# Kernel tuning notes

Hardware: AMD Instinct MI355X
Metric: run time of the kernel (lower is better)

Reference implementation:

```python
import jax, jax.numpy as jnp
import numpy as np

EPS = 1e-8

def setup_inputs() -> dict:
    key = jax.random.key(0)
    k1, k2, k3 = jax.random.split(key, 3)
    b, c, h, w = 64, 20, 128, 128
    x = jax.random.normal(k1, (b, c, h, w), dtype=jnp.float32)
    y = jax.random.randint(k2, (b, c), 0, 2).astype(jnp.int32)
    threshold_p = jnp.zeros((b, c, h * w), dtype=jnp.float32)
    fg = jax.random.uniform(k3, (b, c), dtype=jnp.float32)
    return {"x": x, "y": y, "threshold_p": threshold_p, "fg": fg, "iter": 0}

def reference(x, y, threshold_p, fg, iter):
    b, c, h, w = x.shape
    hw = h * w
    xs = jax.nn.sigmoid(x.reshape(b, c, hw))  # [b,c,hw]
    yf = y.astype(xs.dtype)
    if iter % 100 < 80:
        # per-row descending sort, pick the fg*(h*w)-th value as threshold
        srt = -jnp.sort(-xs.reshape(b * c, hw), axis=1)  # descending
        idx = (fg.reshape(-1) * hw).astype(jnp.int32)  # [b*c]
        thr = jnp.take_along_axis(srt, idx[:, None], axis=1).reshape(b, c, 1)
        thr = jax.lax.stop_gradient(thr)
    else:
        thr = jax.nn.sigmoid(jnp.mean(threshold_p.reshape(b, c, hw), axis=2))[:, :, None]
        xs = jax.lax.stop_gradient(xs)
    thr = jnp.clip(thr, 0.0001)  # [b,c,1], broadcasts over hw
    y_ = yf[:, :, None]  # [b,c,1] broadcast equivalent of stacking hw copies
    mask_low = jax.lax.stop_gradient((xs <= thr).astype(xs.dtype) * y_)
    mask_high = jax.lax.stop_gradient((xs > thr).astype(xs.dtype) * y_)
    h_low = (-(xs * xs) / (thr * thr) + 2.0 * xs / thr) * mask_low
    alpha = 1.0 / jnp.clip((1.0 - thr) ** 2, EPS)
    h_high = alpha * (1.0 - xs) * (1.0 - 2.0 * thr + xs) * mask_high
    if iter % 100 < 80:
        neg_loss = -(1.0 - y_) * jnp.log(jnp.clip(1.0 - xs, EPS))
        loss = jnp.mean(h_high + h_low + neg_loss)
    else:
        loss = jnp.sum(h_low) / jnp.sum(mask_low) + jnp.sum(h_high) / jnp.sum(mask_high)
    return loss
```

## Files before the change

kernel.cpp:

```cpp
#include <hip/hip_runtime.h>

#define HW     16384
#define NROWS  1280
#define NT     512
#define NWAVES (NT / 64)
#define CAP    1024
#define NBIN1  4096

__device__ __forceinline__ unsigned f2u(float f) {
    unsigned u = __float_as_uint(f);
    unsigned m = (unsigned)((int)u >> 31);
    return u ^ (m | 0x80000000u);
}
__device__ __forceinline__ float u2f(unsigned u) {
    u = (u & 0x80000000u) ? (u & 0x7fffffffu) : ~u;
    return __uint_as_float(u);
}

__device__ __forceinline__ void block_scan_pick(
    const unsigned* h, int bpl, int stride, unsigned kk,
    volatile unsigned* s_bin, volatile unsigned* s_k, unsigned* wtot)
{
    const int tid  = threadIdx.x;
    const int lane = tid & 63;
    const int wid  = tid >> 6;
    const int base = tid * bpl;
    unsigned local = 0;
    for (int j = 0; j < bpl; ++j) {
        int b = base + j;
        local += h[stride * b] + (stride == 2 ? h[stride * b + 1] : 0u);
    }
    unsigned s = local;
    #pragma unroll
    for (int off = 1; off < 64; off <<= 1) {
        unsigned t = __shfl_down(s, off, 64);
        if (lane + off < 64) s += t;
    }
    if (lane == 0) wtot[wid] = s;
    __syncthreads();
    unsigned aw = 0;
    #pragma unroll
    for (int w = 0; w < NWAVES; ++w) if (w > wid) aw += wtot[w];
    const unsigned above = aw + (s - local);
    if (above <= kk && above + local > kk) {
        unsigned run = above;
        for (int j = bpl - 1; j >= 0; --j) {
            int b = base + j;
            unsigned c = h[stride * b] + (stride == 2 ? h[stride * b + 1] : 0u);
            if (run + c > kk) { *s_bin = (unsigned)b; *s_k = kk - run; break; }
            run += c;
        }
    }
    __syncthreads();
}

__global__ __launch_bounds__(NT) void spatial_bce_row(
    const float* __restrict__ x, const int* __restrict__ y,
    const float* __restrict__ fg, double* __restrict__ partial)
{
    __shared__ unsigned hist[NBIN1 * 2];
    __shared__ unsigned buf[CAP];
    __shared__ unsigned wtot[NWAVES];
    __shared__ unsigned s_cnt, s_bin, s_k;
    __shared__ float    swf[NWAVES][5];
    __shared__ double   swd[NWAVES];

    const int row  = blockIdx.x;
    const int tid  = threadIdx.x;
    const int lane = tid & 63;
    const int wid  = tid >> 6;
    const float4* x4 = (const float4*)(x + (size_t)row * HW);
    const float L2E   = 1.44269504f;
    const float LN2   = 0.69314718f;
    const float NLCAP = 18.420680744f;

    const int yrow = y[row];

    if (yrow == 0) {
        float a0 = 0.f, a1 = 0.f, a2 = 0.f, a3 = 0.f;
        for (int i = tid; i < HW / 4; i += NT) {
            float4 v = x4[i];
            a0 += fminf(fmaxf(v.x, 0.f) + LN2 * log2f(1.f + exp2f(-L2E * fabsf(v.x))), NLCAP);
            a1 += fminf(fmaxf(v.y, 0.f) + LN2 * log2f(1.f + exp2f(-L2E * fabsf(v.y))), NLCAP);
            a2 += fminf(fmaxf(v.z, 0.f) + LN2 * log2f(1.f + exp2f(-L2E * fabsf(v.z))), NLCAP);
            a3 += fminf(fmaxf(v.w, 0.f) + LN2 * log2f(1.f + exp2f(-L2E * fabsf(v.w))), NLCAP);
        }
        double acc = (double)((a0 + a1) + (a2 + a3));
        #pragma unroll
        for (int off = 32; off > 0; off >>= 1) acc += __shfl_down(acc, off, 64);
        if (lane == 0) swd[wid] = acc;
        __syncthreads();
        if (tid == 0) {
            double t = 0.0;
            for (int w = 0; w < NWAVES; ++w) t += swd[w];
            partial[row] = t;
        }
        return;
    }

    {
        uint4 z = {0u, 0u, 0u, 0u};
        for (int i = tid; i < NBIN1 * 2 / 4; i += NT) ((uint4*)hist)[i] = z;
    }
    if (tid == 0) {
        int k = (int)(fg[row] * (float)HW);
        k = max(0, min(HW - 1, k));
        s_k = (unsigned)k; s_cnt = 0u;
    }
    __syncthreads();
    const unsigned k0 = s_k;

    const int rep = tid & 1;
    for (int i = tid; i < HW / 4; i += 2 * NT) {
        float4 v0 = x4[i];
        float4 v1 = x4[i + NT];
        atomicAdd(&hist[2 * (f2u(v0.x) >> 20) + rep], 1u);
        atomicAdd(&hist[2 * (f2u(v0.y) >> 20) + rep], 1u);
        atomicAdd(&hist[2 * (f2u(v0.z) >> 20) + rep], 1u);
        atomicAdd(&hist[2 * (f2u(v0.w) >> 20) + rep], 1u);
        atomicAdd(&hist[2 * (f2u(v1.x) >> 20) + rep], 1u);
        atomicAdd(&hist[2 * (f2u(v1.y) >> 20) + rep], 1u);
        atomicAdd(&hist[2 * (f2u(v1.z) >> 20) + rep], 1u);
        atomicAdd(&hist[2 * (f2u(v1.w) >> 20) + rep], 1u);
    }
    __syncthreads();
    block_scan_pick(hist, NBIN1 / NT, 2, k0, &s_bin, &s_k, wtot);
    const unsigned bin1 = s_bin;
    const unsigned k1   = s_k;

    for (int i = tid; i < 2048; i += NT) hist[i] = 0u;
    float sLa = 0.f, s2La = 0.f, sHa = 0.f, s2Ha = 0.f;
    float sLb = 0.f, s2Lb = 0.f, sHb = 0.f, s2Hb = 0.f;
    int   nH = 0;
    for (int i = tid; i < HW / 4; i += 2 * NT) {
        float4 v0 = x4[i];
        float4 v1 = x4[i + NT];
        float e0[4] = {v0.x, v0.y, v0.z, v0.w};
        float e1[4] = {v1.x, v1.y, v1.z, v1.w};
        #pragma unroll
        for (int j = 0; j < 4; ++j) {
            float xv = e0[j];
            unsigned u = f2u(xv);
            unsigned b = u >> 20;
            if (b == bin1) {
                unsigned p = atomicAdd(&s_cnt, 1u);
                if (p < CAP) buf[p] = u;
            } else {
                float s = __builtin_amdgcn_rcpf(1.f + exp2f(-L2E * xv));
                float s2 = s * s;
                if (b > bin1) { sHa += s; s2Ha += s2; ++nH; }
                else          { sLa += s; s2La += s2; }
            }
        }
        #pragma unroll
        for (int j = 0; j < 4; ++j) {
            float xv = e1[j];
            unsigned u = f2u(xv);
            unsigned b = u >> 20;
            if (b == bin1) {
                unsigned p = atomicAdd(&s_cnt, 1u);
                if (p < CAP) buf[p] = u;
            } else {
                float s = __builtin_amdgcn_rcpf(1.f + exp2f(-L2E * xv));
                float s2 = s * s;
                if (b > bin1) { sHb += s; s2Hb += s2; ++nH; }
                else          { sLb += s; s2Lb += s2; }
            }
        }
    }
    float sL = sLa + sLb, s2L = s2La + s2Lb;
    float sH = sHa + sHb, s2H = s2Ha + s2Hb;
    __syncthreads();
    const unsigned cnt = s_cnt;

    unsigned ustar;
    if (cnt <= CAP) {
        for (int c = tid; c < (int)cnt; c += NT)
            atomicAdd(&hist[(buf[c] >> 10) & 1023u], 1u);
        __syncthreads();
        block_scan_pick(hist, 1024 / NT, 1, k1, &s_bin, &s_k, wtot);
        const unsigned pfx22 = (bin1 << 10) | s_bin;
        const unsigned k2    = s_k;
        for (int c = tid; c < (int)cnt; c += NT)
            if ((buf[c] >> 10) == pfx22) atomicAdd(&hist[1024 + (buf[c] & 1023u)], 1u);
        __syncthreads();
        block_scan_pick(hist + 1024, 1024 / NT, 1, k2, &s_bin, &s_k, wtot);
        ustar = (pfx22 << 10) | s_bin;
    } else {
        for (int i = tid; i < HW / 4; i += NT) {
            float4 v = x4[i];
            unsigned u[4] = {f2u(v.x), f2u(v.y), f2u(v.z), f2u(v.w)};
            #pragma unroll
            for (int j = 0; j < 4; ++j)
                if ((u[j] >> 20) == bin1) atomicAdd(&hist[(u[j] >> 10) & 1023u], 1u);
        }
        __syncthreads();
        block_scan_pick(hist, 1024 / NT, 1, k1, &s_bin, &s_k, wtot);
        const unsigned pfx22 = (bin1 << 10) | s_bin;
        const unsigned k2    = s_k;
        for (int i = tid; i < HW / 4; i += NT) {
            float4 v = x4[i];
            unsigned u[4] = {f2u(v.x), f2u(v.y), f2u(v.z), f2u(v.w)};
            #pragma unroll
            for (int j = 0; j < 4; ++j)
                if ((u[j] >> 10) == pfx22) atomicAdd(&hist[1024 + (u[j] & 1023u)], 1u);
        }
        __syncthreads();
        block_scan_pick(hist + 1024, 1024 / NT, 1, k2, &s_bin, &s_k, wtot);
        ustar = (pfx22 << 10) | s_bin;
    }

    const float xk = u2f(ustar);
    float thr = 1.0f / (1.0f + expf(-xk));
    thr = fmaxf(thr, 1e-4f);

    if (cnt <= CAP) {
        for (int c = tid; c < (int)cnt; c += NT) {
            float xv = u2f(buf[c]);
            float s  = __builtin_amdgcn_rcpf(1.f + exp2f(-L2E * xv));
            float s2 = s * s;
            if (s > thr) { sH += s; s2H += s2; ++nH; }
            else         { sL += s; s2L += s2; }
        }
    } else {
        for (int i = tid; i < HW / 4; i += NT) {
            float4 v = x4[i];
            float e[4] = {v.x, v.y, v.z, v.w};
            #pragma unroll
            for (int j = 0; j < 4; ++j) {
                unsigned u = f2u(e[j]);
                if ((u >> 20) == bin1) {
                    float s  = __builtin_amdgcn_rcpf(1.f + exp2f(-L2E * e[j]));
                    float s2 = s * s;
                    if (s > thr) { sH += s; s2H += s2; ++nH; }
                    else         { sL += s; s2L += s2; }
                }
            }
        }
    }

    float nHf = (float)nH;
    #pragma unroll
    for (int off = 32; off > 0; off >>= 1) {
        sL  += __shfl_down(sL,  off, 64);
        s2L += __shfl_down(s2L, off, 64);
        sH  += __shfl_down(sH,  off, 64);
        s2H += __shfl_down(s2H, off, 64);
        nHf += __shfl_down(nHf, off, 64);
    }
    if (lane == 0) {
        swf[wid][0] = sL; swf[wid][1] = s2L; swf[wid][2] = sH;
        swf[wid][3] = s2H; swf[wid][4] = nHf;
    }
    __syncthreads();
    if (tid == 0) {
        double SL = 0, S2L = 0, SH = 0, S2H = 0, NH = 0;
        for (int w = 0; w < NWAVES; ++w) {
            SL += swf[w][0]; S2L += swf[w][1]; SH += swf[w][2];
            S2H += swf[w][3]; NH += (double)swf[w][4];
        }
        const double t   = (double)thr;
        const double omt = 1.0 - t;
        const double al  = 1.0 / fmax(omt * omt, 1e-8);
        partial[row] = 2.0 * SL / t - S2L / (t * t)
                     + al * (NH * (1.0 - 2.0 * t) + 2.0 * t * SH - S2H);
    }
}

__global__ __launch_bounds__(256) void spatial_bce_final(
    const double* __restrict__ partial, float* __restrict__ out)
{
    __shared__ double sred[256];
    double acc = 0.0;
    for (int i = threadIdx.x; i < NROWS; i += 256) acc += partial[i];
    sred[threadIdx.x] = acc;
    __syncthreads();
    for (int off = 128; off > 0; off >>= 1) {
        if (threadIdx.x < off) sred[threadIdx.x] += sred[threadIdx.x + off];
        __syncthreads();
    }
    if (threadIdx.x == 0)
        out[0] = (float)(sred[0] / ((double)NROWS * (double)HW));
}

extern "C" void kernel_launch(void* const* d_in, const int* in_sizes, int n_in,
                              void* d_out, int out_size, void* d_ws, size_t ws_size,
                              hipStream_t stream) {
    const float* x  = (const float*)d_in[0];
    const int*   y  = (const int*)d_in[1];
    const float* fg = (const float*)d_in[3];

    double* partial = (double*)d_ws;

    spatial_bce_row<<<NROWS, NT, 0, stream>>>(x, y, fg, partial);
    spatial_bce_final<<<1, 256, 0, stream>>>(partial, (float*)d_out);
}
```

Before: 38.24 us.

## Predict top-k threshold window from Gaussian quantile to skip the histogram pass

For rows with y=1, the coarse 4096-bin histogram pass is replaced by an analytic guess of the k-th order statistic, assuming normal data, via an inverse-normal approximation with a 6-sigma window. One fused pass now accumulates total sigmoid sums, the sums above the window, and counts above and below it, and buffers the in-window candidates. The exact threshold is then found with a small fine histogram and a rank-select over a second buffer. Totals are used to derive the low-side sums. If the window misses k or overflows the buffer, it falls back to the exact radix-select over the whole row, which costs more when the data is not Gaussian-like.

After: 38.38 us. About the same (+0.3%).

```diff
diff --git a/kernel.cpp b/kernel.cpp
--- a/kernel.cpp
+++ b/kernel.cpp
@@ -4,8 +4,8 @@
 #define NROWS  1280
 #define NT     512
 #define NWAVES (NT / 64)
-#define CAP    1024
-#define NBIN1  4096
+#define CAP    1536
+#define MAXB   128
 
 __device__ __forceinline__ unsigned f2u(float f) {
     unsigned u = __float_as_uint(f);
@@ -17,8 +17,37 @@
     return __uint_as_float(u);
 }
 
+__device__ __forceinline__ float norminv(float p) {
+    const float a1=-3.969683028665376e+01f,a2=2.209460984245205e+02f,
+                a3=-2.759285104469687e+02f,a4=1.383577518672690e+02f,
+                a5=-3.066479806614716e+01f,a6=2.506628277459239e+00f;
+    const float b1=-5.447609879822406e+01f,b2=1.615858368580409e+02f,
+                b3=-1.556989798598866e+02f,b4=6.680131188771972e+01f,
+                b5=-1.328068155288572e+01f;
+    const float c1=-7.784894002430293e-03f,c2=-3.223964580411365e-01f,
+                c3=-2.400758277161838e+00f,c4=-2.549732539343734e+00f,
+                c5=4.374664141464968e+00f,c6=2.938163982698783e+00f;
+    const float d1=7.784695709041462e-03f,d2=3.224671290700398e-01f,
+                d3=2.445134137142996e+00f,d4=3.754408661907416e+00f;
+    const float plow = 0.02425f;
+    float q, r;
+    if (p < plow) {
+        q = sqrtf(-2.f * logf(p));
+        return (((((c1*q+c2)*q+c3)*q+c4)*q+c5)*q+c6) /
+               ((((d1*q+d2)*q+d3)*q+d4)*q+1.f);
+    } else if (p <= 1.f - plow) {
+        q = p - 0.5f; r = q * q;
+        return (((((a1*r+a2)*r+a3)*r+a4)*r+a5)*r+a6)*q /
+               (((((b1*r+b2)*r+b3)*r+b4)*r+b5)*r+1.f);
+    } else {
+        q = sqrtf(-2.f * logf(1.f - p));
+        return -(((((c1*q+c2)*q+c3)*q+c4)*q+c5)*q+c6) /
+                ((((d1*q+d2)*q+d3)*q+d4)*q+1.f);
+    }
+}
+
 __device__ __forceinline__ void block_scan_pick(
-    const unsigned* h, int bpl, int stride, unsigned kk,
+    const unsigned* h, int bpl, unsigned kk,
     volatile unsigned* s_bin, volatile unsigned* s_k, unsigned* wtot)
 {
     const int tid  = threadIdx.x;
@@ -26,10 +55,7 @@
     const int wid  = tid >> 6;
     const int base = tid * bpl;
     unsigned local = 0;
-    for (int j = 0; j < bpl; ++j) {
-        int b = base + j;
-        local += h[stride * b] + (stride == 2 ? h[stride * b + 1] : 0u);
-    }
+    for (int j = 0; j < bpl; ++j) local += h[base + j];
     unsigned s = local;
     #pragma unroll
     for (int off = 1; off < 64; off <<= 1) {
@@ -45,9 +71,8 @@
     if (above <= kk && above + local > kk) {
         unsigned run = above;
         for (int j = bpl - 1; j >= 0; --j) {
-            int b = base + j;
-            unsigned c = h[stride * b] + (stride == 2 ? h[stride * b + 1] : 0u);
-            if (run + c > kk) { *s_bin = (unsigned)b; *s_k = kk - run; break; }
+            unsigned c = h[base + j];
+            if (run + c > kk) { *s_bin = (unsigned)(base + j); *s_k = kk - run; break; }
             run += c;
         }
     }
@@ -58,11 +83,12 @@
     const float* __restrict__ x, const int* __restrict__ y,
     const float* __restrict__ fg, double* __restrict__ partial)
 {
-    __shared__ unsigned hist[NBIN1 * 2];
+    __shared__ unsigned hist[4096];
     __shared__ unsigned buf[CAP];
+    __shared__ unsigned buf2[MAXB];
     __shared__ unsigned wtot[NWAVES];
-    __shared__ unsigned s_cnt, s_bin, s_k;
-    __shared__ float    swf[NWAVES][5];
+    __shared__ unsigned s_cnt, s_cnt2, s_bin, s_k, s_val;
+    __shared__ float    swf[NWAVES][6];
     __shared__ double   swd[NWAVES];
 
     const int row  = blockIdx.x;
@@ -98,40 +124,26 @@
         return;
     }
 
+    int k = (int)(fg[row] * (float)HW);
+    k = max(0, min(HW - 1, k));
+    const unsigned ku = (unsigned)k;
+    const float pq  = 1.f - ((float)k + 0.5f) * (1.f / (float)HW);
+    const float z   = norminv(pq);
+    const float phi = 0.39894228f * exp2f(-0.72134752f * z * z);
+    const float sig = sqrtf(pq * (1.f - pq) * (1.f / (float)HW)) / phi;
+    const float dl  = 6.f * sig + 0.02f;
+    const float fa  = z + dl, fb = z - dl;
+    const unsigned ua = f2u(fa), ub = f2u(fb);
+
     {
-        uint4 z = {0u, 0u, 0u, 0u};
-        for (int i = tid; i < NBIN1 * 2 / 4; i += NT) ((uint4*)hist)[i] = z;
-    }
-    if (tid == 0) {
-        int k = (int)(fg[row] * (float)HW);
-        k = max(0, min(HW - 1, k));
-        s_k = (unsigned)k; s_cnt = 0u;
-    }
-    __syncthreads();
-    const unsigned k0 = s_k;
-
-    const int rep = tid & 1;
-    for (int i = tid; i < HW / 4; i += 2 * NT) {
-        float4 v0 = x4[i];
-        float4 v1 = x4[i + NT];
-        atomicAdd(&hist[2 * (f2u(v0.x) >> 20) + rep], 1u);
-        atomicAdd(&hist[2 * (f2u(v0.y) >> 20) + rep], 1u);
-        atomicAdd(&hist[2 * (f2u(v0.z) >> 20) + rep], 1u);
-        atomicAdd(&hist[2 * (f2u(v0.w) >> 20) + rep], 1u);
-        atomicAdd(&hist[2 * (f2u(v1.x) >> 20) + rep], 1u);
-        atomicAdd(&hist[2 * (f2u(v1.y) >> 20) + rep], 1u);
-        atomicAdd(&hist[2 * (f2u(v1.z) >> 20) + rep], 1u);
-        atomicAdd(&hist[2 * (f2u(v1.w) >> 20) + rep], 1u);
-    }
-    __syncthreads();
-    block_scan_pick(hist, NBIN1 / NT, 2, k0, &s_bin, &s_k, wtot);
-    const unsigned bin1 = s_bin;
-    const unsigned k1   = s_k;
-
-    for (int i = tid; i < 2048; i += NT) hist[i] = 0u;
-    float sLa = 0.f, s2La = 0.f, sHa = 0.f, s2Ha = 0.f;
-    float sLb = 0.f, s2Lb = 0.f, sHb = 0.f, s2Hb = 0.f;
-    int   nH = 0;
+        uint4 zz = {0u, 0u, 0u, 0u};
+        for (int i = tid; i < 1024 / 4; i += NT) ((uint4*)hist)[i] = zz;
+    }
+    if (tid == 0) { s_cnt = 0u; s_cnt2 = 0u; }
+    __syncthreads();
+
+    float t1a = 0.f, t2a = 0.f, gaa = 0.f, g2aa = 0.f, cafa = 0.f, cbfa = 0.f;
+    float t1b = 0.f, t2b = 0.f, gab = 0.f, g2ab = 0.f, cafb = 0.f, cbfb = 0.f;
     for (int i = tid; i < HW / 4; i += 2 * NT) {
         float4 v0 = x4[i];
         float4 v1 = x4[i + NT];
@@ -141,52 +153,151 @@
         for (int j = 0; j < 4; ++j) {
             float xv = e0[j];
             unsigned u = f2u(xv);
-            unsigned b = u >> 20;
-            if (b == bin1) {
-                unsigned p = atomicAdd(&s_cnt, 1u);
-                if (p < CAP) buf[p] = u;
-            } else {
-                float s = __builtin_amdgcn_rcpf(1.f + exp2f(-L2E * xv));
-                float s2 = s * s;
-                if (b > bin1) { sHa += s; s2Ha += s2; ++nH; }
-                else          { sLa += s; s2La += s2; }
+            float s = __builtin_amdgcn_rcpf(1.f + exp2f(-L2E * xv));
+            float s2 = s * s;
+            t1a += s; t2a += s2;
+            if (u > ua) { gaa += s; g2aa += s2; cafa += 1.f; }
+            if (u > ub) {
+                cbfa += 1.f;
+                if (u <= ua) { unsigned p = atomicAdd(&s_cnt, 1u); if (p < CAP) buf[p] = u; }
             }
         }
         #pragma unroll
         for (int j = 0; j < 4; ++j) {
             float xv = e1[j];
             unsigned u = f2u(xv);
-            unsigned b = u >> 20;
-            if (b == bin1) {
-                unsigned p = atomicAdd(&s_cnt, 1u);
-                if (p < CAP) buf[p] = u;
-            } else {
-                float s = __builtin_amdgcn_rcpf(1.f + exp2f(-L2E * xv));
-                float s2 = s * s;
-                if (b > bin1) { sHb += s; s2Hb += s2; ++nH; }
-                else          { sLb += s; s2Lb += s2; }
-            }
-        }
-    }
-    float sL = sLa + sLb, s2L = s2La + s2Lb;
-    float sH = sHa + sHb, s2H = s2Ha + s2Hb;
-    __syncthreads();
+            float s = __builtin_amdgcn_rcpf(1.f + exp2f(-L2E * xv));
+            float s2 = s * s;
+            t1b += s; t2b += s2;
+            if (u > ua) { gab += s; g2ab += s2; cafb += 1.f; }
+            if (u > ub) {
+                cbfb += 1.f;
+                if (u <= ua) { unsigned p = atomicAdd(&s_cnt, 1u); if (p < CAP) buf[p] = u; }
+            }
+        }
+    }
+    float t1 = t1a + t1b, t2 = t2a + t2b;
+    float ga = gaa + gab, g2a = g2aa + g2ab;
+    float caf = cafa + cafb, cbf = cbfa + cbfb;
+    #pragma unroll
+    for (int off = 32; off > 0; off >>= 1) {
+        t1  += __shfl_down(t1,  off, 64);
+        t2  += __shfl_down(t2,  off, 64);
+        ga  += __shfl_down(ga,  off, 64);
+        g2a += __shfl_down(g2a, off, 64);
+        caf += __shfl_down(caf, off, 64);
+        cbf += __shfl_down(cbf, off, 64);
+    }
+    if (lane == 0) {
+        swf[wid][0] = t1;  swf[wid][1] = t2;  swf[wid][2] = ga;
+        swf[wid][3] = g2a; swf[wid][4] = caf; swf[wid][5] = cbf;
+    }
+    __syncthreads();
+    double dS1 = 0, dS2 = 0, dGa = 0, dG2a = 0, dCa = 0, dCb = 0;
+    #pragma unroll
+    for (int w = 0; w < NWAVES; ++w) {
+        dS1 += swf[w][0]; dS2 += swf[w][1]; dGa  += swf[w][2];
+        dG2a += swf[w][3]; dCa += swf[w][4]; dCb += swf[w][5];
+    }
+    const unsigned ca  = (unsigned)(dCa + 0.5);
+    const unsigned cb  = (unsigned)(dCb + 0.5);
     const unsigned cnt = s_cnt;
+    const unsigned UCLIP = f2u(-9.2102404f);
+    const bool valid = (ca <= ku) && (ku < cb) && (cnt <= CAP);
 
     unsigned ustar;
-    if (cnt <= CAP) {
-        for (int c = tid; c < (int)cnt; c += NT)
-            atomicAdd(&hist[(buf[c] >> 10) & 1023u], 1u);
-        __syncthreads();
-        block_scan_pick(hist, 1024 / NT, 1, k1, &s_bin, &s_k, wtot);
-        const unsigned pfx22 = (bin1 << 10) | s_bin;
-        const unsigned k2    = s_k;
-        for (int c = tid; c < (int)cnt; c += NT)
-            if ((buf[c] >> 10) == pfx22) atomicAdd(&hist[1024 + (buf[c] & 1023u)], 1u);
-        __syncthreads();
-        block_scan_pick(hist + 1024, 1024 / NT, 1, k2, &s_bin, &s_k, wtot);
-        ustar = (pfx22 << 10) | s_bin;
+    bool addSide;
+    float hs = 0.f, hs2 = 0.f, hn = 0.f;
+
+    if (valid) {
+        const float scale = 1024.f / (fa - fb);
+        for (int c = tid; c < (int)cnt; c += NT) {
+            float xv = u2f(buf[c]);
+            int bn = (int)((xv - fb) * scale);
+            bn = max(0, min(1023, bn));
+            atomicAdd(&hist[bn], 1u);
+        }
+        __syncthreads();
+        const unsigned kp = ku - ca;
+        block_scan_pick(hist, 1024 / NT, kp, &s_bin, &s_k, wtot);
+        const unsigned binv = s_bin;
+        const unsigned kin  = s_k;
+        for (int c = tid; c < (int)cnt; c += NT) {
+            unsigned u = buf[c];
+            float xv = u2f(u);
+            int bn = (int)((xv - fb) * scale);
+            bn = max(0, min(1023, bn));
+            if (bn == (int)binv) { unsigned p = atomicAdd(&s_cnt2, 1u); if (p < MAXB) buf2[p] = u; }
+        }
+        __syncthreads();
+        const unsigned m = s_cnt2;
+        if (m <= MAXB) {
+            for (int i = tid; i < (int)m; i += NT) {
+                unsigned v = buf2[i];
+                unsigned gt = 0, eq = 0;
+                for (int j = 0; j < (int)m; ++j) {
+                    unsigned w = buf2[j];
+                    gt += (w > v); eq += (w == v);
+                }
+                if (gt <= kin && kin < gt + eq) s_val = v;
+            }
+        } else {
+            for (int c = tid; c < (int)cnt; c += NT) {
+                unsigned v = buf[c];
+                unsigned gt = 0, eq = 0;
+                for (int j = 0; j < (int)cnt; ++j) {
+                    unsigned w = buf[j];
+                    gt += (w > v); eq += (w == v);
+                }
+                if (gt <= kp && kp < gt + eq) s_val = v;
+            }
+        }
+        __syncthreads();
+        ustar = s_val;
+
+        if (ustar >= UCLIP) {
+            addSide = true;
+            for (int c = tid; c < (int)cnt; c += NT) {
+                unsigned u = buf[c];
+                if (u > ustar) {
+                    float xv = u2f(u);
+                    float s = __builtin_amdgcn_rcpf(1.f + exp2f(-L2E * xv));
+                    hs += s; hs2 += s * s; hn += 1.f;
+                }
+            }
+        } else {
+            addSide = false;
+            for (int i = tid; i < HW / 4; i += NT) {
+                float4 v = x4[i];
+                float e[4] = {v.x, v.y, v.z, v.w};
+                #pragma unroll
+                for (int j = 0; j < 4; ++j) {
+                    if (f2u(e[j]) > UCLIP) {
+                        float s = __builtin_amdgcn_rcpf(1.f + exp2f(-L2E * e[j]));
+                        hs += s; hs2 += s * s; hn += 1.f;
+                    }
+                }
+            }
+        }
     } else {
+        {
+            uint4 zz = {0u, 0u, 0u, 0u};
+            for (int i = tid; i < 4096 / 4; i += NT) ((uint4*)hist)[i] = zz;
+        }
+        __syncthreads();
+        for (int i = tid; i < HW / 4; i += NT) {
+            float4 v = x4[i];
+            atomicAdd(&hist[f2u(v.x) >> 20], 1u);
+            atomicAdd(&hist[f2u(v.y) >> 20], 1u);
+            atomicAdd(&hist[f2u(v.z) >> 20], 1u);
+            atomicAdd(&hist[f2u(v.w) >> 20], 1u);
+        }
+        __syncthreads();
+        block_scan_pick(hist, 4096 / NT, ku, &s_bin, &s_k, wtot);
+        const unsigned bin1 = s_bin;
+        const unsigned k1   = s_k;
+        for (int i = tid; i < 2048; i += NT) hist[i] = 0u;
+        __syncthreads();
         for (int i = tid; i < HW / 4; i += NT) {
             float4 v = x4[i];
             unsigned u[4] = {f2u(v.x), f2u(v.y), f2u(v.z), f2u(v.w)};
@@ -195,7 +306,7 @@
                 if ((u[j] >> 20) == bin1) atomicAdd(&hist[(u[j] >> 10) & 1023u], 1u);
         }
         __syncthreads();
-        block_scan_pick(hist, 1024 / NT, 1, k1, &s_bin, &s_k, wtot);
+        block_scan_pick(hist, 1024 / NT, k1, &s_bin, &s_k, wtot);
         const unsigned pfx22 = (bin1 << 10) | s_bin;
         const unsigned k2    = s_k;
         for (int i = tid; i < HW / 4; i += NT) {
@@ -206,60 +317,46 @@
                 if ((u[j] >> 10) == pfx22) atomicAdd(&hist[1024 + (u[j] & 1023u)], 1u);
         }
         __syncthreads();
-        block_scan_pick(hist + 1024, 1024 / NT, 1, k2, &s_bin, &s_k, wtot);
+        block_scan_pick(hist + 1024, 1024 / NT, k2, &s_bin, &s_k, wtot);
         ustar = (pfx22 << 10) | s_bin;
-    }
-
-    const float xk = u2f(ustar);
-    float thr = 1.0f / (1.0f + expf(-xk));
-    thr = fmaxf(thr, 1e-4f);
-
-    if (cnt <= CAP) {
-        for (int c = tid; c < (int)cnt; c += NT) {
-            float xv = u2f(buf[c]);
-            float s  = __builtin_amdgcn_rcpf(1.f + exp2f(-L2E * xv));
-            float s2 = s * s;
-            if (s > thr) { sH += s; s2H += s2; ++nH; }
-            else         { sL += s; s2L += s2; }
-        }
-    } else {
+
+        addSide = false;
+        const unsigned uthr = max(ustar, UCLIP);
         for (int i = tid; i < HW / 4; i += NT) {
             float4 v = x4[i];
             float e[4] = {v.x, v.y, v.z, v.w};
             #pragma unroll
             for (int j = 0; j < 4; ++j) {
-                unsigned u = f2u(e[j]);
-                if ((u >> 20) == bin1) {
-                    float s  = __builtin_amdgcn_rcpf(1.f + exp2f(-L2E * e[j]));
-                    float s2 = s * s;
-                    if (s > thr) { sH += s; s2H += s2; ++nH; }
-                    else         { sL += s; s2L += s2; }
-                }
-            }
-        }
-    }
-
-    float nHf = (float)nH;
+                if (f2u(e[j]) > uthr) {
+                    float s = __builtin_amdgcn_rcpf(1.f + exp2f(-L2E * e[j]));
+                    hs += s; hs2 += s * s; hn += 1.f;
+                }
+            }
+        }
+    }
+
     #pragma unroll
     for (int off = 32; off > 0; off >>= 1) {
-        sL  += __shfl_down(sL,  off, 64);
-        s2L += __shfl_down(s2L, off, 64);
-        sH  += __shfl_down(sH,  off, 64);
-        s2H += __shfl_down(s2H, off, 64);
-        nHf += __shfl_down(nHf, off, 64);
-    }
-    if (lane == 0) {
-        swf[wid][0] = sL; swf[wid][1] = s2L; swf[wid][2] = sH;
-        swf[wid][3] = s2H; swf[wid][4] = nHf;
-    }
+        hs  += __shfl_down(hs,  off, 64);
+        hs2 += __shfl_down(hs2, off, 64);
+        hn  += __shfl_down(hn,  off, 64);
+    }
+    if (lane == 0) { swf[wid][0] = hs; swf[wid][1] = hs2; swf[wid][2] = hn; }
     __syncthreads();
     if (tid == 0) {
-        double SL = 0, S2L = 0, SH = 0, S2H = 0, NH = 0;
+        double HS = 0, HS2 = 0, HN = 0;
         for (int w = 0; w < NWAVES; ++w) {
-            SL += swf[w][0]; S2L += swf[w][1]; SH += swf[w][2];
-            S2H += swf[w][3]; NH += (double)swf[w][4];
-        }
-        const double t   = (double)thr;
+            HS += swf[w][0]; HS2 += swf[w][1]; HN += swf[w][2];
+        }
+        double SH, S2H, NH;
+        if (addSide) { SH = dGa + HS; S2H = dG2a + HS2; NH = dCa + HN; }
+        else         { SH = HS;       S2H = HS2;        NH = HN; }
+        const double SL = dS1 - SH, S2L = dS2 - S2H;
+
+        const float xk = u2f(ustar);
+        float thrf = 1.0f / (1.0f + expf(-xk));
+        thrf = fmaxf(thrf, 1e-4f);
+        const double t   = (double)thrf;
         const double omt = 1.0 - t;
         const double al  = 1.0 / fmax(omt * omt, 1e-8);
         partial[row] = 2.0 * SL / t - S2L / (t * t)
```

## Fuse final reduction via last-block counter and unroll row loads by four

Applied to the files above, without the earlier changes.

Removes the separate final reduction kernel: each row block increments a global done counter after a fence, and the last block to finish sums all partials and writes the output. A memset of the counter is added to the stream before the launch. Separately, the load loops in the negative-row, histogram and classification passes now issue four float4 loads per iteration instead of one or two, for more memory-level parallelism. The trade is a small memset launch in place of the second kernel, plus higher register pressure from the unrolling.

Result: slower. 70.55 us (+84.5%).

```diff
diff --git a/kernel.cpp b/kernel.cpp
--- a/kernel.cpp
+++ b/kernel.cpp
@@ -56,12 +56,13 @@
 
 __global__ __launch_bounds__(NT) void spatial_bce_row(
     const float* __restrict__ x, const int* __restrict__ y,
-    const float* __restrict__ fg, double* __restrict__ partial)
+    const float* __restrict__ fg, double* __restrict__ partial,
+    unsigned* __restrict__ done, float* __restrict__ out)
 {
     __shared__ unsigned hist[NBIN1 * 2];
     __shared__ unsigned buf[CAP];
     __shared__ unsigned wtot[NWAVES];
-    __shared__ unsigned s_cnt, s_bin, s_k;
+    __shared__ unsigned s_cnt, s_bin, s_k, s_last;
     __shared__ float    swf[NWAVES][5];
     __shared__ double   swd[NWAVES];
 
@@ -78,12 +79,27 @@
 
     if (yrow == 0) {
         float a0 = 0.f, a1 = 0.f, a2 = 0.f, a3 = 0.f;
-        for (int i = tid; i < HW / 4; i += NT) {
-            float4 v = x4[i];
-            a0 += fminf(fmaxf(v.x, 0.f) + LN2 * log2f(1.f + exp2f(-L2E * fabsf(v.x))), NLCAP);
-            a1 += fminf(fmaxf(v.y, 0.f) + LN2 * log2f(1.f + exp2f(-L2E * fabsf(v.y))), NLCAP);
-            a2 += fminf(fmaxf(v.z, 0.f) + LN2 * log2f(1.f + exp2f(-L2E * fabsf(v.z))), NLCAP);
-            a3 += fminf(fmaxf(v.w, 0.f) + LN2 * log2f(1.f + exp2f(-L2E * fabsf(v.w))), NLCAP);
+        for (int i = tid; i < HW / 4; i += 4 * NT) {
+            float4 v0 = x4[i];
+            float4 v1 = x4[i + NT];
+            float4 v2 = x4[i + 2 * NT];
+            float4 v3 = x4[i + 3 * NT];
+            a0 += fminf(fmaxf(v0.x, 0.f) + LN2 * log2f(1.f + exp2f(-L2E * fabsf(v0.x))), NLCAP);
+            a1 += fminf(fmaxf(v0.y, 0.f) + LN2 * log2f(1.f + exp2f(-L2E * fabsf(v0.y))), NLCAP);
+            a2 += fminf(fmaxf(v0.z, 0.f) + LN2 * log2f(1.f + exp2f(-L2E * fabsf(v0.z))), NLCAP);
+            a3 += fminf(fmaxf(v0.w, 0.f) + LN2 * log2f(1.f + exp2f(-L2E * fabsf(v0.w))), NLCAP);
+            a0 += fminf(fmaxf(v1.x, 0.f) + LN2 * log2f(1.f + exp2f(-L2E * fabsf(v1.x))), NLCAP);
+            a1 += fminf(fmaxf(v1.y, 0.f) + LN2 * log2f(1.f + exp2f(-L2E * fabsf(v1.y))), NLCAP);
+            a2 += fminf(fmaxf(v1.z, 0.f) + LN2 * log2f(1.f + exp2f(-L2E * fabsf(v1.z))), NLCAP);
+            a3 += fminf(fmaxf(v1.w, 0.f) + LN2 * log2f(1.f + exp2f(-L2E * fabsf(v1.w))), NLCAP);
+            a0 += fminf(fmaxf(v2.x, 0.f) + LN2 * log2f(1.f + exp2f(-L2E * fabsf(v2.x))), NLCAP);
+            a1 += fminf(fmaxf(v2.y, 0.f) + LN2 * log2f(1.f + exp2f(-L2E * fabsf(v2.y))), NLCAP);
+            a2 += fminf(fmaxf(v2.z, 0.f) + LN2 * log2f(1.f + exp2f(-L2E * fabsf(v2.z))), NLCAP);
+            a3 += fminf(fmaxf(v2.w, 0.f) + LN2 * log2f(1.f + exp2f(-L2E * fabsf(v2.w))), NLCAP);
+            a0 += fminf(fmaxf(v3.x, 0.f) + LN2 * log2f(1.f + exp2f(-L2E * fabsf(v3.x))), NLCAP);
+            a1 += fminf(fmaxf(v3.y, 0.f) + LN2 * log2f(1.f + exp2f(-L2E * fabsf(v3.y))), NLCAP);
+            a2 += fminf(fmaxf(v3.z, 0.f) + LN2 * log2f(1.f + exp2f(-L2E * fabsf(v3.z))), NLCAP);
+            a3 += fminf(fmaxf(v3.w, 0.f) + LN2 * log2f(1.f + exp2f(-L2E * fabsf(v3.w))), NLCAP);
         }
         double acc = (double)((a0 + a1) + (a2 + a3));
         #pragma unroll
@@ -95,192 +111,209 @@
             for (int w = 0; w < NWAVES; ++w) t += swd[w];
             partial[row] = t;
         }
-        return;
-    }
-
-    {
-        uint4 z = {0u, 0u, 0u, 0u};
-        for (int i = tid; i < NBIN1 * 2 / 4; i += NT) ((uint4*)hist)[i] = z;
-    }
-    if (tid == 0) {
-        int k = (int)(fg[row] * (float)HW);
-        k = max(0, min(HW - 1, k));
-        s_k = (unsigned)k; s_cnt = 0u;
-    }
-    __syncthreads();
-    const unsigned k0 = s_k;
-
-    const int rep = tid & 1;
-    for (int i = tid; i < HW / 4; i += 2 * NT) {
-        float4 v0 = x4[i];
-        float4 v1 = x4[i + NT];
-        atomicAdd(&hist[2 * (f2u(v0.x) >> 20) + rep], 1u);
-        atomicAdd(&hist[2 * (f2u(v0.y) >> 20) + rep], 1u);
-        atomicAdd(&hist[2 * (f2u(v0.z) >> 20) + rep], 1u);
-        atomicAdd(&hist[2 * (f2u(v0.w) >> 20) + rep], 1u);
-        atomicAdd(&hist[2 * (f2u(v1.x) >> 20) + rep], 1u);
-        atomicAdd(&hist[2 * (f2u(v1.y) >> 20) + rep], 1u);
-        atomicAdd(&hist[2 * (f2u(v1.z) >> 20) + rep], 1u);
-        atomicAdd(&hist[2 * (f2u(v1.w) >> 20) + rep], 1u);
-    }
-    __syncthreads();
-    block_scan_pick(hist, NBIN1 / NT, 2, k0, &s_bin, &s_k, wtot);
-    const unsigned bin1 = s_bin;
-    const unsigned k1   = s_k;
-
-    for (int i = tid; i < 2048; i += NT) hist[i] = 0u;
-    float sLa = 0.f, s2La = 0.f, sHa = 0.f, s2Ha = 0.f;
-    float sLb = 0.f, s2Lb = 0.f, sHb = 0.f, s2Hb = 0.f;
-    int   nH = 0;
-    for (int i = tid; i < HW / 4; i += 2 * NT) {
-        float4 v0 = x4[i];
-        float4 v1 = x4[i + NT];
-        float e0[4] = {v0.x, v0.y, v0.z, v0.w};
-        float e1[4] = {v1.x, v1.y, v1.z, v1.w};
+    } else {
+        {
+            uint4 z = {0u, 0u, 0u, 0u};
+            for (int i = tid; i < NBIN1 * 2 / 4; i += NT) ((uint4*)hist)[i] = z;
+        }
+        if (tid == 0) {
+            int k = (int)(fg[row] * (float)HW);
+            k = max(0, min(HW - 1, k));
+            s_k = (unsigned)k; s_cnt = 0u;
+        }
+        __syncthreads();
+        const unsigned k0 = s_k;
+
+        const int rep = tid & 1;
+        for (int i = tid; i < HW / 4; i += 4 * NT) {
+            float4 v0 = x4[i];
+            float4 v1 = x4[i + NT];
+            float4 v2 = x4[i + 2 * NT];
+            float4 v3 = x4[i + 3 * NT];
+            atomicAdd(&hist[2 * (f2u(v0.x) >> 20) + rep], 1u);
+            atomicAdd(&hist[2 * (f2u(v0.y) >> 20) + rep], 1u);
+            atomicAdd(&hist[2 * (f2u(v0.z) >> 20) + rep], 1u);
+            atomicAdd(&hist[2 * (f2u(v0.w) >> 20) + rep], 1u);
+            atomicAdd(&hist[2 * (f2u(v1.x) >> 20) + rep], 1u);
+            atomicAdd(&hist[2 * (f2u(v1.y) >> 20) + rep], 1u);
+            atomicAdd(&hist[2 * (f2u(v1.z) >> 20) + rep], 1u);
+            atomicAdd(&hist[2 * (f2u(v1.w) >> 20) + rep], 1u);
+            atomicAdd(&hist[2 * (f2u(v2.x) >> 20) + rep], 1u);
+            atomicAdd(&hist[2 * (f2u(v2.y) >> 20) + rep], 1u);
+            atomicAdd(&hist[2 * (f2u(v2.z) >> 20) + rep], 1u);
+            atomicAdd(&hist[2 * (f2u(v2.w) >> 20) + rep], 1u);
+            atomicAdd(&hist[2 * (f2u(v3.x) >> 20) + rep], 1u);
+            atomicAdd(&hist[2 * (f2u(v3.y) >> 20) + rep], 1u);
+            atomicAdd(&hist[2 * (f2u(v3.z) >> 20) + rep], 1u);
+            atomicAdd(&hist[2 * (f2u(v3.w) >> 20) + rep], 1u);
+        }
+        __syncthreads();
+        block_scan_pick(hist, NBIN1 / NT, 2, k0, &s_bin, &s_k, wtot);
+        const unsigned bin1 = s_bin;
+        const unsigned k1   = s_k;
+
+        for (int i = tid; i < 2048; i += NT) hist[i] = 0u;
+        float sLa = 0.f, s2La = 0.f, sHa = 0.f, s2Ha = 0.f;
+        float sLb = 0.f, s2Lb = 0.f, sHb = 0.f, s2Hb = 0.f;
+        int   nH = 0;
+        for (int i = tid; i < HW / 4; i += 4 * NT) {
+            float4 v0 = x4[i];
+            float4 v1 = x4[i + NT];
+            float4 v2 = x4[i + 2 * NT];
+            float4 v3 = x4[i + 3 * NT];
+            float e0[8] = {v0.x, v0.y, v0.z, v0.w, v1.x, v1.y, v1.z, v1.w};
+            float e1[8] = {v2.x, v2.y, v2.z, v2.w, v3.x, v3.y, v3.z, v3.w};
+            #pragma unroll
+            for (int j = 0; j < 8; ++j) {
+                float xv = e0[j];
+                unsigned u = f2u(xv);
+                unsigned b = u >> 20;
+                if (b == bin1) {
+                    unsigned p = atomicAdd(&s_cnt, 1u);
+                    if (p < CAP) buf[p] = u;
+                } else {
+                    float s = __builtin_amdgcn_rcpf(1.f + exp2f(-L2E * xv));
+                    float s2 = s * s;
+                    if (b > bin1) { sHa += s; s2Ha += s2; ++nH; }
+                    else          { sLa += s; s2La += s2; }
+                }
+            }
+            #pragma unroll
+            for (int j = 0; j < 8; ++j) {
+                float xv = e1[j];
+                unsigned u = f2u(xv);
+                unsigned b = u >> 20;
+                if (b == bin1) {
+                    unsigned p = atomicAdd(&s_cnt, 1u);
+                    if (p < CAP) buf[p] = u;
+                } else {
+                    float s = __builtin_amdgcn_rcpf(1.f + exp2f(-L2E * xv));
+                    float s2 = s * s;
+                    if (b > bin1) { sHb += s; s2Hb += s2; ++nH; }
+                    else          { sLb += s; s2Lb += s2; }
+                }
+            }
+        }
+        float sL = sLa + sLb, s2L = s2La + s2Lb;
+        float sH = sHa + sHb, s2H = s2Ha + s2Hb;
+        __syncthreads();
+        const unsigned cnt = s_cnt;
+
+        unsigned ustar;
+        if (cnt <= CAP) {
+            for (int c = tid; c < (int)cnt; c += NT)
+                atomicAdd(&hist[(buf[c] >> 10) & 1023u], 1u);
+            __syncthreads();
+            block_scan_pick(hist, 1024 / NT, 1, k1, &s_bin, &s_k, wtot);
+            const unsigned pfx22 = (bin1 << 10) | s_bin;
+            const unsigned k2    = s_k;
+            for (int c = tid; c < (int)cnt; c += NT)
+                if ((buf[c] >> 10) == pfx22) atomicAdd(&hist[1024 + (buf[c] & 1023u)], 1u);
+            __syncthreads();
+            block_scan_pick(hist + 1024, 1024 / NT, 1, k2, &s_bin, &s_k, wtot);
+            ustar = (pfx22 << 10) | s_bin;
+        } else {
+            for (int i = tid; i < HW / 4; i += NT) {
+                float4 v = x4[i];
+                unsigned u[4] = {f2u(v.x), f2u(v.y), f2u(v.z), f2u(v.w)};
+                #pragma unroll
+                for (int j = 0; j < 4; ++j)
+                    if ((u[j] >> 20) == bin1) atomicAdd(&hist[(u[j] >> 10) & 1023u], 1u);
+            }
+            __syncthreads();
+            block_scan_pick(hist, 1024 / NT, 1, k1, &s_bin, &s_k, wtot);
+            const unsigned pfx22 = (bin1 << 10) | s_bin;
+            const unsigned k2    = s_k;
+            for (int i = tid; i < HW / 4; i += NT) {
+                float4 v = x4[i];
+                unsigned u[4] = {f2u(v.x), f2u(v.y), f2u(v.z), f2u(v.w)};
+                #pragma unroll
+                for (int j = 0; j < 4; ++j)
+                    if ((u[j] >> 10) == pfx22) atomicAdd(&hist[1024 + (u[j] & 1023u)], 1u);
+            }
+            __syncthreads();
+            block_scan_pick(hist + 1024, 1024 / NT, 1, k2, &s_bin, &s_k, wtot);
+            ustar = (pfx22 << 10) | s_bin;
+        }
+
+        const float xk = u2f(ustar);
+        float thr = 1.0f / (1.0f + expf(-xk));
+        thr = fmaxf(thr, 1e-4f);
+
+        if (cnt <= CAP) {
+            for (int c = tid; c < (int)cnt; c += NT) {
+                float xv = u2f(buf[c]);
+                float s  = __builtin_amdgcn_rcpf(1.f + exp2f(-L2E * xv));
+                float s2 = s * s;
+                if (s > thr) { sH += s; s2H += s2; ++nH; }
+                else         { sL += s; s2L += s2; }
+            }
+        } else {
+            for (int i = tid; i < HW / 4; i += NT) {
+                float4 v = x4[i];
+                float e[4] = {v.x, v.y, v.z, v.w};
+                #pragma unroll
+                for (int j = 0; j < 4; ++j) {
+                    unsigned u = f2u(e[j]);
+                    if ((u >> 20) == bin1) {
+                        float s  = __builtin_amdgcn_rcpf(1.f + exp2f(-L2E * e[j]));
+                        float s2 = s * s;
+                        if (s > thr) { sH += s; s2H += s2; ++nH; }
+                        else         { sL += s; s2L += s2; }
+                    }
+                }
+            }
+        }
+
+        float nHf = (float)nH;
         #pragma unroll
-        for (int j = 0; j < 4; ++j) {
-            float xv = e0[j];
-            unsigned u = f2u(xv);
-            unsigned b = u >> 20;
-            if (b == bin1) {
-                unsigned p = atomicAdd(&s_cnt, 1u);
-                if (p < CAP) buf[p] = u;
-            } else {
-                float s = __builtin_amdgcn_rcpf(1.f + exp2f(-L2E * xv));
-                float s2 = s * s;
-                if (b > bin1) { sHa += s; s2Ha += s2; ++nH; }
-                else          { sLa += s; s2La += s2; }
-            }
-        }
-        #pragma unroll
-        for (int j = 0; j < 4; ++j) {
-            float xv = e1[j];
-            unsigned u = f2u(xv);
-            unsigned b = u >> 20;
-            if (b == bin1) {
-                unsigned p = atomicAdd(&s_cnt, 1u);
-                if (p < CAP) buf[p] = u;
-            } else {
-                float s = __builtin_amdgcn_rcpf(1.f + exp2f(-L2E * xv));
-                float s2 = s * s;
-                if (b > bin1) { sHb += s; s2Hb += s2; ++nH; }
-                else          { sLb += s; s2Lb += s2; }
-            }
-        }
-    }
-    float sL = sLa + sLb, s2L = s2La + s2Lb;
-    float sH = sHa + sHb, s2H = s2Ha + s2Hb;
-    __syncthreads();
-    const unsigned cnt = s_cnt;
-
-    unsigned ustar;
-    if (cnt <= CAP) {
-        for (int c = tid; c < (int)cnt; c += NT)
-            atomicAdd(&hist[(buf[c] >> 10) & 1023u], 1u);
-        __syncthreads();
-        block_scan_pick(hist, 1024 / NT, 1, k1, &s_bin, &s_k, wtot);
-        const unsigned pfx22 = (bin1 << 10) | s_bin;
-        const unsigned k2    = s_k;
-        for (int c = tid; c < (int)cnt; c += NT)
-            if ((buf[c] >> 10) == pfx22) atomicAdd(&hist[1024 + (buf[c] & 1023u)], 1u);
-        __syncthreads();
-        block_scan_pick(hist + 1024, 1024 / NT, 1, k2, &s_bin, &s_k, wtot);
-        ustar = (pfx22 << 10) | s_bin;
-    } else {
-        for (int i = tid; i < HW / 4; i += NT) {
-            float4 v = x4[i];
-            unsigned u[4] = {f2u(v.x), f2u(v.y), f2u(v.z), f2u(v.w)};
-            #pragma unroll
-            for (int j = 0; j < 4; ++j)
-                if ((u[j] >> 20) == bin1) atomicAdd(&hist[(u[j] >> 10) & 1023u], 1u);
-        }
-        __syncthreads();
-        block_scan_pick(hist, 1024 / NT, 1, k1, &s_bin, &s_k, wtot);
-        const unsigned pfx22 = (bin1 << 10) | s_bin;
-        const unsigned k2    = s_k;
-        for (int i = tid; i < HW / 4; i += NT) {
-            float4 v = x4[i];
-            unsigned u[4] = {f2u(v.x), f2u(v.y), f2u(v.z), f2u(v.w)};
-            #pragma unroll
-            for (int j = 0; j < 4; ++j)
-                if ((u[j] >> 10) == pfx22) atomicAdd(&hist[1024 + (u[j] & 1023u)], 1u);
-        }
-        __syncthreads();
-        block_scan_pick(hist + 1024, 1024 / NT, 1, k2, &s_bin, &s_k, wtot);
-        ustar = (pfx22 << 10) | s_bin;
-    }
-
-    const float xk = u2f(ustar);
-    float thr = 1.0f / (1.0f + expf(-xk));
-    thr = fmaxf(thr, 1e-4f);
-
-    if (cnt <= CAP) {
-        for (int c = tid; c < (int)cnt; c += NT) {
-            float xv = u2f(buf[c]);
-            float s  = __builtin_amdgcn_rcpf(1.f + exp2f(-L2E * xv));
-            float s2 = s * s;
-            if (s > thr) { sH += s; s2H += s2; ++nH; }
-            else         { sL += s; s2L += s2; }
-        }
-    } else {
-        for (int i = tid; i < HW / 4; i += NT) {
-            float4 v = x4[i];
-            float e[4] = {v.x, v.y, v.z, v.w};
-            #pragma unroll
-            for (int j = 0; j < 4; ++j) {
-                unsigned u = f2u(e[j]);
-                if ((u >> 20) == bin1) {
-                    float s  = __builtin_amdgcn_rcpf(1.f + exp2f(-L2E * e[j]));
-                    float s2 = s * s;
-                    if (s > thr) { sH += s; s2H += s2; ++nH; }
-                    else         { sL += s; s2L += s2; }
-                }
-            }
-        }
-    }
-
-    float nHf = (float)nH;
-    #pragma unroll
-    for (int off = 32; off > 0; off >>= 1) {
-        sL  += __shfl_down(sL,  off, 64);
-        s2L += __shfl_down(s2L, off, 64);
-        sH  += __shfl_down(sH,  off, 64);
-        s2H += __shfl_down(s2H, off, 64);
-        nHf += __shfl_down(nHf, off, 64);
-    }
-    if (lane == 0) {
-        swf[wid][0] = sL; swf[wid][1] = s2L; swf[wid][2] = sH;
-        swf[wid][3] = s2H; swf[wid][4] = nHf;
-    }
+        for (int off = 32; off > 0; off >>= 1) {
+            sL  += __shfl_down(sL,  off, 64);
+            s2L += __shfl_down(s2L, off, 64);
+            sH  += __shfl_down(sH,  off, 64);
+            s2H += __shfl_down(s2H, off, 64);
+            nHf += __shfl_down(nHf, off, 64);
+        }
+        if (lane == 0) {
+            swf[wid][0] = sL; swf[wid][1] = s2L; swf[wid][2] = sH;
+            swf[wid][3] = s2H; swf[wid][4] = nHf;
+        }
+        __syncthreads();
+        if (tid == 0) {
+            double SL = 0, S2L = 0, SH = 0, S2H = 0, NH = 0;
+            for (int w = 0; w < NWAVES; ++w) {
+                SL += swf[w][0]; S2L += swf[w][1]; SH += swf[w][2];
+                S2H += swf[w][3]; NH += (double)swf[w][4];
+            }
+            const double t   = (double)thr;
+            const double omt = 1.0 - t;
+            const double al  = 1.0 / fmax(omt * omt, 1e-8);
+            partial[row] = 2.0 * SL / t - S2L / (t * t)
+                         + al * (NH * (1.0 - 2.0 * t) + 2.0 * t * SH - S2H);
+        }
+    }
+
     __syncthreads();
     if (tid == 0) {
-        double SL = 0, S2L = 0, SH = 0, S2H = 0, NH = 0;
-        for (int w = 0; w < NWAVES; ++w) {
-            SL += swf[w][0]; S2L += swf[w][1]; SH += swf[w][2];
-            S2H += swf[w][3]; NH += (double)swf[w][4];
-        }
-        const double t   = (double)thr;
-        const double omt = 1.0 - t;
-        const double al  = 1.0 / fmax(omt * omt, 1e-8);
-        partial[row] = 2.0 * SL / t - S2L / (t * t)
-                     + al * (NH * (1.0 - 2.0 * t) + 2.0 * t * SH - S2H);
-    }
-}
-
-__global__ __launch_bounds__(256) void spatial_bce_final(
-    const double* __restrict__ partial, float* __restrict__ out)
-{
-    __shared__ double sred[256];
-    double acc = 0.0;
-    for (int i = threadIdx.x; i < NROWS; i += 256) acc += partial[i];
-    sred[threadIdx.x] = acc;
+        __threadfence();
+        unsigned old = atomicAdd(done, 1u);
+        s_last = (old == NROWS - 1) ? 1u : 0u;
+    }
     __syncthreads();
-    for (int off = 128; off > 0; off >>= 1) {
-        if (threadIdx.x < off) sred[threadIdx.x] += sred[threadIdx.x + off];
-        __syncthreads();
-    }
-    if (threadIdx.x == 0)
-        out[0] = (float)(sred[0] / ((double)NROWS * (double)HW));
+    if (s_last) {
+        __threadfence();
+        double* sred = (double*)hist;
+        double a = 0.0;
+        for (int i = tid; i < NROWS; i += NT) a += partial[i];
+        sred[tid] = a;
+        __syncthreads();
+        for (int off = NT / 2; off > 0; off >>= 1) {
+            if (tid < off) sred[tid] += sred[tid + off];
+            __syncthreads();
+        }
+        if (tid == 0)
+            out[0] = (float)(sred[0] / ((double)NROWS * (double)HW));
+    }
 }
 
 extern "C" void kernel_launch(void* const* d_in, const int* in_sizes, int n_in,
@@ -290,8 +323,10 @@
     const int*   y  = (const int*)d_in[1];
     const float* fg = (const float*)d_in[3];
 
-    double* partial = (double*)d_ws;
-
-    spatial_bce_row<<<NROWS, NT, 0, stream>>>(x, y, fg, partial);
-    spatial_bce_final<<<1, 256, 0, stream>>>(partial, (float*)d_out);
-}
+    double*   partial = (double*)d_ws;
+    unsigned* done    = (unsigned*)((char*)d_ws + (size_t)NROWS * 8);
+
+    hipMemsetAsync(done, 0, sizeof(unsigned), stream);
+    spatial_bce_row<<<NROWS, NT, 0, stream>>>(x, y, fg, partial, done,
+                                              (float*)d_out);
+}
```
